# Performance work log

Measured on AMD Instinct MI355X. Metric: run time of the kernel, lower is better.

Reference implementation:

```python
import jax, jax.numpy as jnp
import numpy as np

N_HEAD, DK, DV = 16, 64, 64
TEMP = DK ** 0.5
LN_EPS = 1e-5


def setup_inputs() -> dict:
    key = jax.random.key(0)
    ks = jax.random.split(key, 8)
    B, LQ, LK = 8, 1024, 1024
    D1, D2 = 768, 1024
    return {
        'q': jax.random.normal(ks[0], (B, LQ, D1), jnp.float32),
        'k': jax.random.normal(ks[1], (B, LK, D2), jnp.float32),
        'v': jax.random.normal(ks[2], (B, LK, D2), jnp.float32),
        'w_qs': jax.random.normal(ks[3], (D1, N_HEAD * DK), jnp.float32) * 0.02,
        'w_ks': jax.random.normal(ks[4], (D2, N_HEAD * DK), jnp.float32) * 0.02,
        'w_vs': jax.random.normal(ks[5], (D2, N_HEAD * DV), jnp.float32) * 0.02,
        'fc_w': jax.random.normal(ks[6], (N_HEAD * DV, D2), jnp.float32) * 0.02,
        'resid_w': jax.random.normal(ks[7], (D1, N_HEAD * DV), jnp.float32) * 0.02,
        'resid_b': jnp.zeros((N_HEAD * DV,), jnp.float32),
        'ln_gamma': jnp.ones((D2,), jnp.float32),
        'ln_beta': jnp.zeros((D2,), jnp.float32),
    }


def reference(q, k, v, w_qs, w_ks, w_vs, fc_w, resid_w, resid_b, ln_gamma, ln_beta):
    B, LQ, _ = q.shape
    LK = k.shape[1]
    residual = q
    # project and split heads: [B, L, H, d] -> [B, H, L, d]
    Q = (q @ w_qs).reshape(B, LQ, N_HEAD, DK).transpose(0, 2, 1, 3)
    K = (k @ w_ks).reshape(B, LK, N_HEAD, DK).transpose(0, 2, 1, 3)
    V = (v @ w_vs).reshape(B, LK, N_HEAD, DV).transpose(0, 2, 1, 3)
    scores = jnp.einsum('bhqd,bhkd->bhqk', Q / TEMP, K)
    p = jax.nn.softmax(scores, axis=-1)
    # reverse-complement attention (RCA): reverse=True
    p = (1.0 - p) / (LK - 1)
    out = jnp.einsum('bhqk,bhkd->bhqd', p, V)  # dropout is eval-mode identity
    out = out.transpose(0, 2, 1, 3).reshape(B, LQ, N_HEAD * DV)
    out = out @ fc_w
    out = out + (residual @ resid_w + resid_b)
    mean = jnp.mean(out, axis=-1, keepdims=True)
    var = jnp.var(out, axis=-1, keepdims=True)
    out = (out - mean) * jax.lax.rsqrt(var + LN_EPS) * ln_gamma + ln_beta
    return out  # relu=False
```

## Files before the change

kernel.cpp:

```cpp
#include <hip/hip_runtime.h>

typedef __bf16 bf16_t;
typedef __bf16 bf16x8 __attribute__((ext_vector_type(8)));
typedef __bf16 bf16x4 __attribute__((ext_vector_type(4)));
typedef float  f32x4  __attribute__((ext_vector_type(4)));

#if __has_builtin(__builtin_amdgcn_exp2f)
#define EXP2(x) __builtin_amdgcn_exp2f(x)
#else
#define EXP2(x) exp2f(x)
#endif

#define DEVFN __device__ __forceinline__

DEVFN void gl_lds16(void* lds_base, const void* gsrc) {
  __builtin_amdgcn_global_load_lds(
      (const __attribute__((address_space(1))) void*)gsrc,
      (__attribute__((address_space(3))) void*)lds_base, 16, 0, 0);
}

__global__ __launch_bounds__(256) void k_prep(
    const float* __restrict__ q, const float* __restrict__ k, const float* __restrict__ v,
    const float* __restrict__ w_qs, const float* __restrict__ w_ks,
    const float* __restrict__ w_vs, const float* __restrict__ fc_w,
    const float* __restrict__ resid_w,
    bf16_t* __restrict__ qb, bf16_t* __restrict__ kb, bf16_t* __restrict__ vb,
    bf16_t* __restrict__ wqsT, bf16_t* __restrict__ wksT, bf16_t* __restrict__ wvsT,
    bf16_t* __restrict__ fcwT, bf16_t* __restrict__ rswT,
    float* __restrict__ Vs) {
  __shared__ float t[64][65];
  int bid = blockIdx.x;
  if (bid < 1152) {
    const float* w; bf16_t* wt; int K;
    if (bid < 192)      { w = w_qs;    wt = wqsT; K = 768; }
    else if (bid < 448) { w = w_ks;    wt = wksT; K = 1024; bid -= 192; }
    else if (bid < 704) { w = w_vs;    wt = wvsT; K = 1024; bid -= 448; }
    else if (bid < 960) { w = fc_w;    wt = fcwT; K = 1024; bid -= 704; }
    else                { w = resid_w; wt = rswT; K = 768;  bid -= 960; }
    const int bk = (bid >> 4) << 6;
    const int bn = (bid & 15) << 6;
    const int rr = threadIdx.x >> 4;
    const int cc = (threadIdx.x & 15) << 2;
#pragma unroll
    for (int i = 0; i < 4; ++i) {
      int r = i * 16 + rr;
      float4 vv = *reinterpret_cast<const float4*>(&w[(size_t)(bk + r) * 1024 + bn + cc]);
      t[r][cc] = vv.x; t[r][cc + 1] = vv.y; t[r][cc + 2] = vv.z; t[r][cc + 3] = vv.w;
    }
    __syncthreads();
#pragma unroll
    for (int i = 0; i < 4; ++i) {
      int n = i * 16 + rr;
      bf16x4 o;
      o[0] = (bf16_t)t[cc][n];     o[1] = (bf16_t)t[cc + 1][n];
      o[2] = (bf16_t)t[cc + 2][n]; o[3] = (bf16_t)t[cc + 3][n];
      *reinterpret_cast<bf16x4*>(&wt[(size_t)(bn + n) * K + bk + cc]) = o;
    }
    return;
  }
  bid -= 1152;
  if (bid == 0) {
    for (int j = threadIdx.x; j < 8192; j += 256) Vs[j] = 0.f;
  }
  const int NQ = 1572864, NK = 2097152, NT = NQ + 2 * NK;
  int stride = (gridDim.x - 1152) * 256;
  for (int i = bid * 256 + threadIdx.x; i < NT; i += stride) {
    const float* src; bf16_t* dst; int off;
    if (i < NQ)           { src = q; dst = qb; off = i; }
    else if (i < NQ + NK) { src = k; dst = kb; off = i - NQ; }
    else                  { src = v; dst = vb; off = i - NQ - NK; }
    float4 vv = reinterpret_cast<const float4*>(src)[off];
    bf16x4 o;
    o[0] = (bf16_t)vv.x; o[1] = (bf16_t)vv.y; o[2] = (bf16_t)vv.z; o[3] = (bf16_t)vv.w;
    reinterpret_cast<bf16x4*>(dst)[off] = o;
  }
}

DEVFN void gemm_tiles(const bf16_t* __restrict__ A, const bf16_t* __restrict__ Bt,
                      int K, int m0, int n0, bf16_t (*sm)[4096], f32x4 (&acc)[4][4]) {
  const int lane = threadIdx.x & 63;
  const int wv = threadIdx.x >> 6;
  const int wr = (wv >> 1) * 64, wc = (wv & 1) * 64;
  const int lr = lane & 15, lk = lane >> 4;
  const int so0 = wv * 2048 + lane * 16;
  const int so1 = so0 + 1024;
  const int r0 = so0 >> 6, r1 = so1 >> 6;
  const int c0 = ((((so0 >> 4) & 3) ^ ((r0 >> 1) & 3)) << 4);
  const int c1 = ((((so1 >> 4) & 3) ^ ((r1 >> 1) & 3)) << 4);
  const int asw = ((lk ^ ((lr >> 1) & 3)) << 4);
  const char* Apc = (const char*)A;
  const char* Btc = (const char*)Bt;
  f32x4 zro = {0.f, 0.f, 0.f, 0.f};
#pragma unroll
  for (int i = 0; i < 4; ++i)
#pragma unroll
    for (int j = 0; j < 4; ++j) acc[i][j] = zro;

  const int nk = K >> 5;
  auto stage = [&](int buf, int t) {
    gl_lds16((char*)sm[2 * buf]     + wv * 2048,        Apc + ((size_t)(m0 + r0) * K + t * 32) * 2 + c0);
    gl_lds16((char*)sm[2 * buf]     + wv * 2048 + 1024, Apc + ((size_t)(m0 + r1) * K + t * 32) * 2 + c1);
    gl_lds16((char*)sm[2 * buf + 1] + wv * 2048,        Btc + ((size_t)(n0 + r0) * K + t * 32) * 2 + c0);
    gl_lds16((char*)sm[2 * buf + 1] + wv * 2048 + 1024, Btc + ((size_t)(n0 + r1) * K + t * 32) * 2 + c1);
  };
  stage(0, 0);
  if (nk > 1) {
    stage(1, 1);
    asm volatile("s_waitcnt vmcnt(4)" ::: "memory");
  } else {
    asm volatile("s_waitcnt vmcnt(0)" ::: "memory");
  }
  __builtin_amdgcn_s_barrier();

  for (int t = 0; t < nk; ++t) {
    const int cur = t % 3;
    const char* AsB = (const char*)sm[2 * cur];
    const char* BsB = (const char*)sm[2 * cur + 1];
    bf16x8 af[4], bfr[4];
#pragma unroll
    for (int i = 0; i < 4; ++i)
      af[i] = *(const bf16x8*)(AsB + (wr + i * 16 + lr) * 64 + asw);
#pragma unroll
    for (int j = 0; j < 4; ++j)
      bfr[j] = *(const bf16x8*)(BsB + (wc + j * 16 + lr) * 64 + asw);
#pragma unroll
    for (int i = 0; i < 4; ++i)
#pragma unroll
      for (int j = 0; j < 4; ++j)
        acc[i][j] = __builtin_amdgcn_mfma_f32_16x16x32_bf16(af[i], bfr[j], acc[i][j], 0, 0, 0);
    __builtin_amdgcn_s_barrier();
    if (t + 2 < nk) stage((t + 2) % 3, t + 2);
    if (t + 1 < nk) {
      if (t + 2 < nk) asm volatile("s_waitcnt vmcnt(4)" ::: "memory");
      else            asm volatile("s_waitcnt vmcnt(0)" ::: "memory");
      __builtin_amdgcn_s_barrier();
    }
  }
}

__global__ __launch_bounds__(256, 3) void k_gemm_proj(
    const bf16_t* __restrict__ qb, const bf16_t* __restrict__ wqsT, bf16_t* __restrict__ Qp,
    const bf16_t* __restrict__ kb, const bf16_t* __restrict__ wksT, bf16_t* __restrict__ Kp,
    const bf16_t* __restrict__ vb, const bf16_t* __restrict__ wvsT, bf16_t* __restrict__ Vt,
    float* __restrict__ Vsum, float qscale) {
  __shared__ bf16_t sm[6][4096];
  const int bid = blockIdx.x;
  const int route = bid >> 9;
  const int sbid = bid & 511;
  const int wg = (sbid & 7) * 64 + (sbid >> 3);
  const int tn = 8;
  const int m0 = (wg / tn) << 7;
  const int n0 = (wg % tn) << 7;
  const int lane = threadIdx.x & 63;
  const int wv = threadIdx.x >> 6;
  const int wr = (wv >> 1) * 64, wc = (wv & 1) * 64;
  const int lr = lane & 15, lk = lane >> 4;
  f32x4 acc[4][4];

  if (route == 0) {
    gemm_tiles(vb, wvsT, 1024, m0, n0, sm, acc);
    const int b = m0 >> 10;
    const int h0 = n0 >> 6;
    const int kt0 = (m0 & 1023) >> 6;
    const int h_local = wc >> 6, kt_local = wr >> 6;
    char* tl = (char*)sm + (h_local * 2 + kt_local) * 8192;
#pragma unroll
    for (int i = 0; i < 4; ++i) {
      const int kvl = i * 16 + lk * 4;
      const int csel = kvl >> 3;
      const int hoff = (kvl & 7) * 2;
#pragma unroll
      for (int j = 0; j < 4; ++j) {
        const int d = j * 16 + lr;
        bf16x4 pw;
#pragma unroll
        for (int r = 0; r < 4; ++r) pw[r] = (bf16_t)acc[i][j][r];
        *reinterpret_cast<bf16x4*>(tl + d * 128 + ((csel ^ (d & 7)) << 4) + hoff) = pw;
      }
    }
    {
      const size_t gbase = (size_t)(b * 16 + h0 + h_local) * 131072 +
                           (size_t)(kt0 + kt_local) * 8192;
#pragma unroll
      for (int it = 0; it < 8; ++it)
        *reinterpret_cast<uint4*>((char*)Vt + gbase + it * 1024 + lane * 16) =
            *reinterpret_cast<const uint4*>(tl + it * 1024 + lane * 16);
    }
    const int h = h0 + h_local;
#pragma unroll
    for (int j = 0; j < 4; ++j) {
      float s = 0.f;
#pragma unroll
      for (int i = 0; i < 4; ++i)
#pragma unroll
        for (int r = 0; r < 4; ++r) s += acc[i][j][r];
      s += __shfl_xor(s, 16, 64);
      s += __shfl_xor(s, 32, 64);
      if (lane < 16)
        atomicAdd(&Vsum[(b * 16 + h) * 64 + j * 16 + lane], s);
    }
  } else if (route == 1) {
    gemm_tiles(kb, wksT, 1024, m0, n0, sm, acc);
#pragma unroll
    for (int i = 0; i < 4; ++i)
#pragma unroll
      for (int j = 0; j < 4; ++j)
#pragma unroll
        for (int r = 0; r < 4; ++r)
          Kp[(size_t)(m0 + wr + i * 16 + lk * 4 + r) * 1024 + n0 + wc + j * 16 + lr] =
              (bf16_t)acc[i][j][r];
  } else {
    gemm_tiles(qb, wqsT, 768, m0, n0, sm, acc);
#pragma unroll
    for (int i = 0; i < 4; ++i)
#pragma unroll
      for (int j = 0; j < 4; ++j)
#pragma unroll
        for (int r = 0; r < 4; ++r)
          Qp[(size_t)(m0 + wr + i * 16 + lk * 4 + r) * 1024 + n0 + wc + j * 16 + lr] =
              (bf16_t)(acc[i][j][r] * qscale);
  }
}

__global__ __launch_bounds__(256, 3) void k_gemm_final(
    const bf16_t* __restrict__ A1, const bf16_t* __restrict__ B1t, int K1,
    const bf16_t* __restrict__ A2, const bf16_t* __restrict__ B2t, int K2,
    const float* __restrict__ bias, bf16_t* __restrict__ Y, int N) {
  __shared__ bf16_t sm[6][4096];
  const int bpx = gridDim.x >> 3;
  const int wg = (blockIdx.x & 7) * bpx + (blockIdx.x >> 3);
  const int tn = N >> 7;
  const int m0 = (wg / tn) << 7;
  const int n0 = (wg % tn) << 7;
  const int lane = threadIdx.x & 63;
  const int wv = threadIdx.x >> 6;
  const int wr = (wv >> 1) * 64, wc = (wv & 1) * 64;
  const int lr = lane & 15, lk = lane >> 4;
  const int so0 = wv * 2048 + lane * 16;
  const int so1 = so0 + 1024;
  const int r0 = so0 >> 6, r1 = so1 >> 6;
  const int c0 = ((((so0 >> 4) & 3) ^ ((r0 >> 1) & 3)) << 4);
  const int c1 = ((((so1 >> 4) & 3) ^ ((r1 >> 1) & 3)) << 4);
  const int asw = ((lk ^ ((lr >> 1) & 3)) << 4);
  f32x4 zro = {0.f, 0.f, 0.f, 0.f};
  f32x4 acc[4][4];
#pragma unroll
  for (int i = 0; i < 4; ++i)
#pragma unroll
    for (int j = 0; j < 4; ++j) acc[i][j] = zro;

  const int nk1 = K1 >> 5;
  const int nkt = (K1 + K2) >> 5;
  auto stage = [&](int buf, int t) {
    const char* Apc; const char* Btc; int K, tt;
    if (t < nk1) { Apc = (const char*)A1; Btc = (const char*)B1t; K = K1; tt = t; }
    else         { Apc = (const char*)A2; Btc = (const char*)B2t; K = K2; tt = t - nk1; }
    gl_lds16((char*)sm[2 * buf]     + wv * 2048,        Apc + ((size_t)(m0 + r0) * K + tt * 32) * 2 + c0);
    gl_lds16((char*)sm[2 * buf]     + wv * 2048 + 1024, Apc + ((size_t)(m0 + r1) * K + tt * 32) * 2 + c1);
    gl_lds16((char*)sm[2 * buf + 1] + wv * 2048,        Btc + ((size_t)(n0 + r0) * K + tt * 32) * 2 + c0);
    gl_lds16((char*)sm[2 * buf + 1] + wv * 2048 + 1024, Btc + ((size_t)(n0 + r1) * K + tt * 32) * 2 + c1);
  };
  stage(0, 0);
  stage(1, 1);
  asm volatile("s_waitcnt vmcnt(4)" ::: "memory");
  __builtin_amdgcn_s_barrier();
  for (int t = 0; t < nkt; ++t) {
    const int cur = t % 3;
    const char* AsB = (const char*)sm[2 * cur];
    const char* BsB = (const char*)sm[2 * cur + 1];
    bf16x8 af[4], bfr[4];
#pragma unroll
    for (int i = 0; i < 4; ++i)
      af[i] = *(const bf16x8*)(AsB + (wr + i * 16 + lr) * 64 + asw);
#pragma unroll
    for (int j = 0; j < 4; ++j)
      bfr[j] = *(const bf16x8*)(BsB + (wc + j * 16 + lr) * 64 + asw);
#pragma unroll
    for (int i = 0; i < 4; ++i)
#pragma unroll
      for (int j = 0; j < 4; ++j)
        acc[i][j] = __builtin_amdgcn_mfma_f32_16x16x32_bf16(af[i], bfr[j], acc[i][j], 0, 0, 0);
    __builtin_amdgcn_s_barrier();
    if (t + 2 < nkt) stage((t + 2) % 3, t + 2);
    if (t + 1 < nkt) {
      if (t + 2 < nkt) asm volatile("s_waitcnt vmcnt(4)" ::: "memory");
      else             asm volatile("s_waitcnt vmcnt(0)" ::: "memory");
      __builtin_amdgcn_s_barrier();
    }
  }
#pragma unroll
  for (int i = 0; i < 4; ++i)
#pragma unroll
    for (int j = 0; j < 4; ++j) {
      float bv = bias[n0 + wc + j * 16 + lr];
#pragma unroll
      for (int r = 0; r < 4; ++r)
        Y[(size_t)(m0 + wr + i * 16 + lk * 4 + r) * N + n0 + wc + j * 16 + lr] =
            (bf16_t)(acc[i][j][r] + bv);
    }
}

__global__ __launch_bounds__(1024) void k_attn(
    const bf16_t* __restrict__ Qp, const bf16_t* __restrict__ Kp,
    const bf16_t* __restrict__ Vt, const float* __restrict__ Vsum,
    bf16_t* __restrict__ Aout) {
  const int bid = blockIdx.x;
  const int wgid = (bid & 7) * 32 + (bid >> 3);
  const int qg = wgid & 1;
  const int bh = wgid >> 1;
  const int b = bh >> 4, h = bh & 15;
  __shared__ bf16_t Ks[2][4096];
  __shared__ bf16_t Vs[2][4096];
  const int tid = threadIdx.x;
  const int lane = tid & 63;
  const int wv = tid >> 6;
  const int lr = lane & 15, lk = lane >> 4;
  const int stb = (wv >> 2) * 2;
  const int wrow = (wv & 3) * 16;

  const int o = (tid & 511) * 16;
  const int row = o >> 7;
  const int sc = ((((o >> 4) & 7) ^ (row & 7)) << 4);
  const int srow = (row & 0x23) | ((row & 0x0C) << 1) | ((row & 0x10) >> 2);
  const bool isK = tid < 512;

  const char* Ksrc  = (const char*)(Kp + ((size_t)(b * 1024 + srow)) * 1024 + h * 64) + sc;
  const char* Vtile = (const char*)Vt + (size_t)bh * 131072 + o;
  const char* gsrc   = isK ? Ksrc : Vtile;
  const size_t gstep = isK ? (size_t)131072 : (size_t)8192;
  char* l0 = isK ? ((char*)&Ks[0][0] + o) : ((char*)&Vs[0][0] + o);
  char* l1 = isK ? ((char*)&Ks[1][0] + o) : ((char*)&Vs[1][0] + o);

  gl_lds16(l0, gsrc);

  bf16x8 qa[2][2];
#pragma unroll
  for (int stl = 0; stl < 2; ++stl) {
    const char* qsrc = (const char*)(Qp +
        ((size_t)(b * 1024 + qg * 512 + (stb + stl) * 64 + wrow + lr)) * 1024 + h * 64);
    qa[stl][0] = *(const bf16x8*)(qsrc + lk * 16);
    qa[stl][1] = *(const bf16x8*)(qsrc + 64 + lk * 16);
  }
  __syncthreads();

  const int kb0 = lr * 128 + ((lk ^ (lr & 7)) << 4);
  const int kb1 = lr * 128 + (((4 + lk) ^ (lr & 7)) << 4);

  f32x4 zro = {0.f, 0.f, 0.f, 0.f};
  f32x4 oacc[2][4];
  f32x4 sum[2];
#pragma unroll
  for (int stl = 0; stl < 2; ++stl) {
    sum[stl] = zro;
#pragma unroll
    for (int g = 0; g < 4; ++g) oacc[stl][g] = zro;
  }
  bf16x8 ones8;
#pragma unroll
  for (int j = 0; j < 8; ++j) ones8[j] = (bf16_t)1.0f;

  for (int kt = 0; kt < 16; ++kt) {
    const int cur = kt & 1;
    const char* KsB = (const char*)&Ks[cur][0];
    const char* VsB = (const char*)&Vs[cur][0];
    if (kt < 15)
      gl_lds16(cur ? l0 : l1, gsrc + (size_t)(kt + 1) * gstep);

    f32x4 sacc[2][4];
#pragma unroll
    for (int stl = 0; stl < 2; ++stl)
#pragma unroll
      for (int g = 0; g < 4; ++g) sacc[stl][g] = zro;
    {
      bf16x8 kf[4];
#pragma unroll
      for (int g = 0; g < 4; ++g) kf[g] = *(const bf16x8*)(KsB + kb0 + g * 2048);
#pragma unroll
      for (int stl = 0; stl < 2; ++stl)
#pragma unroll
        for (int g = 0; g < 4; ++g)
          sacc[stl][g] = __builtin_amdgcn_mfma_f32_16x16x32_bf16(kf[g], qa[stl][0], sacc[stl][g], 0, 0, 0);
#pragma unroll
      for (int g = 0; g < 4; ++g) kf[g] = *(const bf16x8*)(KsB + kb1 + g * 2048);
#pragma unroll
      for (int stl = 0; stl < 2; ++stl)
#pragma unroll
        for (int g = 0; g < 4; ++g)
          sacc[stl][g] = __builtin_amdgcn_mfma_f32_16x16x32_bf16(kf[g], qa[stl][1], sacc[stl][g], 0, 0, 0);
    }

    bf16x8 pa[2][2];
#pragma unroll
    for (int stl = 0; stl < 2; ++stl)
#pragma unroll
      for (int c = 0; c < 2; ++c) {
        bf16x8 pw;
#pragma unroll
        for (int r = 0; r < 4; ++r) {
          pw[r]     = (bf16_t)EXP2(sacc[stl][2 * c][r]);
          pw[4 + r] = (bf16_t)EXP2(sacc[stl][2 * c + 1][r]);
        }
        pa[stl][c] = pw;
      }

#pragma unroll
    for (int c = 0; c < 2; ++c) {
      const int vb = (c == 0) ? kb0 : kb1;
      bf16x8 vf[4];
#pragma unroll
      for (int gd = 0; gd < 4; ++gd)
        vf[gd] = *(const bf16x8*)(VsB + vb + gd * 2048);
#pragma unroll
      for (int stl = 0; stl < 2; ++stl) {
        sum[stl] = __builtin_amdgcn_mfma_f32_16x16x32_bf16(pa[stl][c], ones8, sum[stl], 0, 0, 0);
#pragma unroll
        for (int gd = 0; gd < 4; ++gd)
          oacc[stl][gd] = __builtin_amdgcn_mfma_f32_16x16x32_bf16(pa[stl][c], vf[gd], oacc[stl][gd], 0, 0, 0);
      }
    }
    __syncthreads();
  }

  float vs_d[4];
#pragma unroll
  for (int gd = 0; gd < 4; ++gd) vs_d[gd] = Vsum[bh * 64 + gd * 16 + lr];
#pragma unroll
  for (int stl = 0; stl < 2; ++stl) {
    float inv[4];
#pragma unroll
    for (int r = 0; r < 4; ++r) inv[r] = 1.0f / sum[stl][r];
#pragma unroll
    for (int gd = 0; gd < 4; ++gd)
#pragma unroll
      for (int r = 0; r < 4; ++r) {
        int d = gd * 16 + lr;
        int qrow = qg * 512 + (stb + stl) * 64 + wrow + lk * 4 + r;
        float attnv = oacc[stl][gd][r] * inv[r];
        float val = (vs_d[gd] - attnv) * (1.0f / 1023.0f);
        Aout[((size_t)(b * 1024 + qrow)) * 1024 + h * 64 + d] = (bf16_t)val;
      }
  }
}

__global__ __launch_bounds__(256) void k_ln(
    const bf16_t* __restrict__ Y, const float* __restrict__ gamma,
    const float* __restrict__ beta, float* __restrict__ out) {
  const int row = blockIdx.x, tid = threadIdx.x;
  bf16x4 xv = reinterpret_cast<const bf16x4*>(Y + (size_t)row * 1024)[tid];
  float x0 = (float)xv[0], x1 = (float)xv[1], x2 = (float)xv[2], x3 = (float)xv[3];
  float s = x0 + x1 + x2 + x3;
  float q = x0 * x0 + x1 * x1 + x2 * x2 + x3 * x3;
#pragma unroll
  for (int off = 32; off > 0; off >>= 1) {
    s += __shfl_xor(s, off, 64);
    q += __shfl_xor(q, off, 64);
  }
  __shared__ float ss[4], qs[4];
  if ((tid & 63) == 0) { ss[tid >> 6] = s; qs[tid >> 6] = q; }
  __syncthreads();
  s = ss[0] + ss[1] + ss[2] + ss[3];
  q = qs[0] + qs[1] + qs[2] + qs[3];
  float mean = s * (1.f / 1024.f);
  float var = q * (1.f / 1024.f) - mean * mean;
  float rstd = rsqrtf(var + 1e-5f);
  float4 g = reinterpret_cast<const float4*>(gamma)[tid];
  float4 bt = reinterpret_cast<const float4*>(beta)[tid];
  float4 o;
  o.x = (x0 - mean) * rstd * g.x + bt.x;
  o.y = (x1 - mean) * rstd * g.y + bt.y;
  o.z = (x2 - mean) * rstd * g.z + bt.z;
  o.w = (x3 - mean) * rstd * g.w + bt.w;
  reinterpret_cast<float4*>(out + (size_t)row * 1024)[tid] = o;
}

extern "C" void kernel_launch(void* const* d_in, const int* in_sizes, int n_in,
                              void* d_out, int out_size, void* d_ws, size_t ws_size,
                              hipStream_t stream) {
  (void)in_sizes; (void)n_in; (void)out_size;
  const float* q       = (const float*)d_in[0];
  const float* k       = (const float*)d_in[1];
  const float* v       = (const float*)d_in[2];
  const float* w_qs    = (const float*)d_in[3];
  const float* w_ks    = (const float*)d_in[4];
  const float* w_vs    = (const float*)d_in[5];
  const float* fc_w    = (const float*)d_in[6];
  const float* resid_w = (const float*)d_in[7];
  const float* resid_b = (const float*)d_in[8];
  const float* ln_g    = (const float*)d_in[9];
  const float* ln_b    = (const float*)d_in[10];
  float* out = (float*)d_out;
  char* ws = (char*)d_ws;

  if (ws_size < (size_t)122716160) return;

  bf16_t* qb   = (bf16_t*)(ws + 0);
  bf16_t* kb   = (bf16_t*)(ws + 12582912);
  bf16_t* vb   = (bf16_t*)(ws + 29360128);
  bf16_t* Y    = (bf16_t*)(ws + 12582912);
  bf16_t* wqsT = (bf16_t*)(ws + 46137344);
  bf16_t* wksT = (bf16_t*)(ws + 47710208);
  bf16_t* wvsT = (bf16_t*)(ws + 49807360);
  bf16_t* fcwT = (bf16_t*)(ws + 51904512);
  bf16_t* rswT = (bf16_t*)(ws + 54001664);
  bf16_t* Qp   = (bf16_t*)(ws + 55574528);
  bf16_t* Kp   = (bf16_t*)(ws + 72351744);
  bf16_t* Aout = (bf16_t*)(ws + 89128960);
  bf16_t* VtT  = (bf16_t*)(ws + 105906176);
  float*  Vsm  = (float*)(ws + 122683392);

  k_prep<<<3200, 256, 0, stream>>>(q, k, v, w_qs, w_ks, w_vs, fc_w, resid_w,
                                   qb, kb, vb, wqsT, wksT, wvsT, fcwT, rswT, Vsm);
  k_gemm_proj<<<1536, 256, 0, stream>>>(qb, wqsT, Qp, kb, wksT, Kp, vb, wvsT, VtT,
                                        Vsm, 0.18033688011f);
  k_attn<<<256, 1024, 0, stream>>>(Qp, Kp, VtT, Vsm, Aout);
  k_gemm_final<<<512, 256, 0, stream>>>(Aout, fcwT, 1024, qb, rswT, 768, resid_b, Y, 1024);
  k_ln<<<8192, 256, 0, stream>>>(Y, ln_g, ln_b, out);
}
```

Baseline: 168.1 us.

## Enlarge GEMM tiles to 256x128 for projection and final GEMMs

Doubles the M dimension of the GEMM block tile from 128 to 256 rows in both the projection and final GEMM kernels. Each wave now computes 128x64 with 8x4 MFMA accumulators, and staging loads 4 A and 2 B chunks per thread into a larger 72KB triple-buffered LDS. The V-transpose epilogue is reworked to write two 64-row tiles per wave. This raises arithmetic intensity and halves the grid, but increases register and LDS pressure and drops the occupancy hint. The final GEMM now gets only 256 blocks, which may underfill the GPU.

Result: slower. 200.9 us (+19.5%).

```diff
diff --git a/kernel.cpp b/kernel.cpp
--- a/kernel.cpp
+++ b/kernel.cpp
@@ -77,121 +77,134 @@
 }
 
 DEVFN void gemm_tiles(const bf16_t* __restrict__ A, const bf16_t* __restrict__ Bt,
-                      int K, int m0, int n0, bf16_t (*sm)[4096], f32x4 (&acc)[4][4]) {
-  const int lane = threadIdx.x & 63;
-  const int wv = threadIdx.x >> 6;
-  const int wr = (wv >> 1) * 64, wc = (wv & 1) * 64;
+                      int K, int m0, int n0, char* sm, f32x4 (&acc)[8][4]) {
+  const int tid = threadIdx.x;
+  const int lane = tid & 63;
+  const int wv = tid >> 6;
+  const int wr = (wv >> 1) * 128, wc = (wv & 1) * 64;
   const int lr = lane & 15, lk = lane >> 4;
-  const int so0 = wv * 2048 + lane * 16;
-  const int so1 = so0 + 1024;
-  const int r0 = so0 >> 6, r1 = so1 >> 6;
-  const int c0 = ((((so0 >> 4) & 3) ^ ((r0 >> 1) & 3)) << 4);
-  const int c1 = ((((so1 >> 4) & 3) ^ ((r1 >> 1) & 3)) << 4);
   const int asw = ((lk ^ ((lr >> 1) & 3)) << 4);
   const char* Apc = (const char*)A;
   const char* Btc = (const char*)Bt;
+
+  int rA[4], cA[4], rB[2], cB[2];
+#pragma unroll
+  for (int it = 0; it < 4; ++it) {
+    int o = tid * 16 + it * 4096;
+    rA[it] = o >> 6;
+    cA[it] = ((((o >> 4) & 3) ^ ((rA[it] >> 1) & 3)) << 4);
+  }
+#pragma unroll
+  for (int it = 0; it < 2; ++it) {
+    int o = tid * 16 + it * 4096;
+    rB[it] = o >> 6;
+    cB[it] = ((((o >> 4) & 3) ^ ((rB[it] >> 1) & 3)) << 4);
+  }
+
   f32x4 zro = {0.f, 0.f, 0.f, 0.f};
 #pragma unroll
-  for (int i = 0; i < 4; ++i)
+  for (int i = 0; i < 8; ++i)
 #pragma unroll
     for (int j = 0; j < 4; ++j) acc[i][j] = zro;
 
   const int nk = K >> 5;
   auto stage = [&](int buf, int t) {
-    gl_lds16((char*)sm[2 * buf]     + wv * 2048,        Apc + ((size_t)(m0 + r0) * K + t * 32) * 2 + c0);
-    gl_lds16((char*)sm[2 * buf]     + wv * 2048 + 1024, Apc + ((size_t)(m0 + r1) * K + t * 32) * 2 + c1);
-    gl_lds16((char*)sm[2 * buf + 1] + wv * 2048,        Btc + ((size_t)(n0 + r0) * K + t * 32) * 2 + c0);
-    gl_lds16((char*)sm[2 * buf + 1] + wv * 2048 + 1024, Btc + ((size_t)(n0 + r1) * K + t * 32) * 2 + c1);
+    char* base = sm + buf * 24576;
+#pragma unroll
+    for (int it = 0; it < 4; ++it)
+      gl_lds16(base + tid * 16 + it * 4096,
+               Apc + ((size_t)(m0 + rA[it]) * K + t * 32) * 2 + cA[it]);
+#pragma unroll
+    for (int it = 0; it < 2; ++it)
+      gl_lds16(base + 16384 + tid * 16 + it * 4096,
+               Btc + ((size_t)(n0 + rB[it]) * K + t * 32) * 2 + cB[it]);
   };
   stage(0, 0);
-  if (nk > 1) {
-    stage(1, 1);
-    asm volatile("s_waitcnt vmcnt(4)" ::: "memory");
-  } else {
-    asm volatile("s_waitcnt vmcnt(0)" ::: "memory");
-  }
+  stage(1, 1);
+  asm volatile("s_waitcnt vmcnt(6)" ::: "memory");
   __builtin_amdgcn_s_barrier();
 
   for (int t = 0; t < nk; ++t) {
     const int cur = t % 3;
-    const char* AsB = (const char*)sm[2 * cur];
-    const char* BsB = (const char*)sm[2 * cur + 1];
-    bf16x8 af[4], bfr[4];
-#pragma unroll
-    for (int i = 0; i < 4; ++i)
+    const char* AsB = sm + cur * 24576;
+    const char* BsB = AsB + 16384;
+    bf16x8 af[8], bfr[4];
+#pragma unroll
+    for (int i = 0; i < 8; ++i)
       af[i] = *(const bf16x8*)(AsB + (wr + i * 16 + lr) * 64 + asw);
 #pragma unroll
     for (int j = 0; j < 4; ++j)
       bfr[j] = *(const bf16x8*)(BsB + (wc + j * 16 + lr) * 64 + asw);
 #pragma unroll
-    for (int i = 0; i < 4; ++i)
+    for (int i = 0; i < 8; ++i)
 #pragma unroll
       for (int j = 0; j < 4; ++j)
         acc[i][j] = __builtin_amdgcn_mfma_f32_16x16x32_bf16(af[i], bfr[j], acc[i][j], 0, 0, 0);
     __builtin_amdgcn_s_barrier();
     if (t + 2 < nk) stage((t + 2) % 3, t + 2);
     if (t + 1 < nk) {
-      if (t + 2 < nk) asm volatile("s_waitcnt vmcnt(4)" ::: "memory");
+      if (t + 2 < nk) asm volatile("s_waitcnt vmcnt(6)" ::: "memory");
       else            asm volatile("s_waitcnt vmcnt(0)" ::: "memory");
       __builtin_amdgcn_s_barrier();
     }
   }
 }
 
-__global__ __launch_bounds__(256, 3) void k_gemm_proj(
+__global__ __launch_bounds__(256) void k_gemm_proj(
     const bf16_t* __restrict__ qb, const bf16_t* __restrict__ wqsT, bf16_t* __restrict__ Qp,
     const bf16_t* __restrict__ kb, const bf16_t* __restrict__ wksT, bf16_t* __restrict__ Kp,
     const bf16_t* __restrict__ vb, const bf16_t* __restrict__ wvsT, bf16_t* __restrict__ Vt,
     float* __restrict__ Vsum, float qscale) {
-  __shared__ bf16_t sm[6][4096];
+  __shared__ __align__(16) char sm[73728];
   const int bid = blockIdx.x;
-  const int route = bid >> 9;
-  const int sbid = bid & 511;
-  const int wg = (sbid & 7) * 64 + (sbid >> 3);
-  const int tn = 8;
-  const int m0 = (wg / tn) << 7;
-  const int n0 = (wg % tn) << 7;
+  const int route = bid >> 8;
+  const int sbid = bid & 255;
+  const int wg = (sbid & 7) * 32 + (sbid >> 3);
+  const int m0 = (wg >> 3) << 8;
+  const int n0 = (wg & 7) << 7;
   const int lane = threadIdx.x & 63;
   const int wv = threadIdx.x >> 6;
-  const int wr = (wv >> 1) * 64, wc = (wv & 1) * 64;
+  const int wr = (wv >> 1) * 128, wc = (wv & 1) * 64;
   const int lr = lane & 15, lk = lane >> 4;
-  f32x4 acc[4][4];
+  f32x4 acc[8][4];
 
   if (route == 0) {
     gemm_tiles(vb, wvsT, 1024, m0, n0, sm, acc);
     const int b = m0 >> 10;
     const int h0 = n0 >> 6;
     const int kt0 = (m0 & 1023) >> 6;
-    const int h_local = wc >> 6, kt_local = wr >> 6;
-    char* tl = (char*)sm + (h_local * 2 + kt_local) * 8192;
-#pragma unroll
-    for (int i = 0; i < 4; ++i) {
-      const int kvl = i * 16 + lk * 4;
+    const int h_local = wc >> 6;
+#pragma unroll
+    for (int i = 0; i < 8; ++i) {
+      const int kvl = (i & 3) * 16 + lk * 4;
       const int csel = kvl >> 3;
       const int hoff = (kvl & 7) * 2;
+      char* slot = sm + (wv * 2 + (i >> 2)) * 8192;
 #pragma unroll
       for (int j = 0; j < 4; ++j) {
         const int d = j * 16 + lr;
         bf16x4 pw;
 #pragma unroll
         for (int r = 0; r < 4; ++r) pw[r] = (bf16_t)acc[i][j][r];
-        *reinterpret_cast<bf16x4*>(tl + d * 128 + ((csel ^ (d & 7)) << 4) + hoff) = pw;
+        *reinterpret_cast<bf16x4*>(slot + d * 128 + ((csel ^ (d & 7)) << 4) + hoff) = pw;
       }
     }
     {
-      const size_t gbase = (size_t)(b * 16 + h0 + h_local) * 131072 +
-                           (size_t)(kt0 + kt_local) * 8192;
-#pragma unroll
-      for (int it = 0; it < 8; ++it)
-        *reinterpret_cast<uint4*>((char*)Vt + gbase + it * 1024 + lane * 16) =
-            *reinterpret_cast<const uint4*>(tl + it * 1024 + lane * 16);
+      const size_t gb = (size_t)(b * 16 + h0 + h_local) * 131072 +
+                        (size_t)(kt0 + (wr >> 6)) * 8192;
+#pragma unroll
+      for (int tl = 0; tl < 2; ++tl)
+#pragma unroll
+        for (int it = 0; it < 8; ++it)
+          *reinterpret_cast<uint4*>((char*)Vt + gb + tl * 8192 + it * 1024 + lane * 16) =
+              *reinterpret_cast<const uint4*>(sm + (wv * 2 + tl) * 8192 + it * 1024 + lane * 16);
     }
     const int h = h0 + h_local;
 #pragma unroll
     for (int j = 0; j < 4; ++j) {
       float s = 0.f;
 #pragma unroll
-      for (int i = 0; i < 4; ++i)
+      for (int i = 0; i < 8; ++i)
 #pragma unroll
         for (int r = 0; r < 4; ++r) s += acc[i][j][r];
       s += __shfl_xor(s, 16, 64);
@@ -202,7 +215,7 @@
   } else if (route == 1) {
     gemm_tiles(kb, wksT, 1024, m0, n0, sm, acc);
 #pragma unroll
-    for (int i = 0; i < 4; ++i)
+    for (int i = 0; i < 8; ++i)
 #pragma unroll
       for (int j = 0; j < 4; ++j)
 #pragma unroll
@@ -212,7 +225,7 @@
   } else {
     gemm_tiles(qb, wqsT, 768, m0, n0, sm, acc);
 #pragma unroll
-    for (int i = 0; i < 4; ++i)
+    for (int i = 0; i < 8; ++i)
 #pragma unroll
       for (int j = 0; j < 4; ++j)
 #pragma unroll
@@ -222,30 +235,40 @@
   }
 }
 
-__global__ __launch_bounds__(256, 3) void k_gemm_final(
+__global__ __launch_bounds__(256) void k_gemm_final(
     const bf16_t* __restrict__ A1, const bf16_t* __restrict__ B1t, int K1,
     const bf16_t* __restrict__ A2, const bf16_t* __restrict__ B2t, int K2,
     const float* __restrict__ bias, bf16_t* __restrict__ Y, int N) {
-  __shared__ bf16_t sm[6][4096];
-  const int bpx = gridDim.x >> 3;
-  const int wg = (blockIdx.x & 7) * bpx + (blockIdx.x >> 3);
-  const int tn = N >> 7;
-  const int m0 = (wg / tn) << 7;
-  const int n0 = (wg % tn) << 7;
-  const int lane = threadIdx.x & 63;
-  const int wv = threadIdx.x >> 6;
-  const int wr = (wv >> 1) * 64, wc = (wv & 1) * 64;
+  __shared__ __align__(16) char sm[73728];
+  const int bid = blockIdx.x;
+  const int wg = (bid & 7) * 32 + (bid >> 3);
+  const int m0 = (wg >> 3) << 8;
+  const int n0 = (wg & 7) << 7;
+  const int tid = threadIdx.x;
+  const int lane = tid & 63;
+  const int wv = tid >> 6;
+  const int wr = (wv >> 1) * 128, wc = (wv & 1) * 64;
   const int lr = lane & 15, lk = lane >> 4;
-  const int so0 = wv * 2048 + lane * 16;
-  const int so1 = so0 + 1024;
-  const int r0 = so0 >> 6, r1 = so1 >> 6;
-  const int c0 = ((((so0 >> 4) & 3) ^ ((r0 >> 1) & 3)) << 4);
-  const int c1 = ((((so1 >> 4) & 3) ^ ((r1 >> 1) & 3)) << 4);
   const int asw = ((lk ^ ((lr >> 1) & 3)) << 4);
+
+  int rA[4], cA[4], rB[2], cB[2];
+#pragma unroll
+  for (int it = 0; it < 4; ++it) {
+    int o = tid * 16 + it * 4096;
+    rA[it] = o >> 6;
+    cA[it] = ((((o >> 4) & 3) ^ ((rA[it] >> 1) & 3)) << 4);
+  }
+#pragma unroll
+  for (int it = 0; it < 2; ++it) {
+    int o = tid * 16 + it * 4096;
+    rB[it] = o >> 6;
+    cB[it] = ((((o >> 4) & 3) ^ ((rB[it] >> 1) & 3)) << 4);
+  }
+
   f32x4 zro = {0.f, 0.f, 0.f, 0.f};
-  f32x4 acc[4][4];
-#pragma unroll
-  for (int i = 0; i < 4; ++i)
+  f32x4 acc[8][4];
+#pragma unroll
+  for (int i = 0; i < 8; ++i)
 #pragma unroll
     for (int j = 0; j < 4; ++j) acc[i][j] = zro;
 
@@ -255,41 +278,46 @@
     const char* Apc; const char* Btc; int K, tt;
     if (t < nk1) { Apc = (const char*)A1; Btc = (const char*)B1t; K = K1; tt = t; }
     else         { Apc = (const char*)A2; Btc = (const char*)B2t; K = K2; tt = t - nk1; }
-    gl_lds16((char*)sm[2 * buf]     + wv * 2048,        Apc + ((size_t)(m0 + r0) * K + tt * 32) * 2 + c0);
-    gl_lds16((char*)sm[2 * buf]     + wv * 2048 + 1024, Apc + ((size_t)(m0 + r1) * K + tt * 32) * 2 + c1);
-    gl_lds16((char*)sm[2 * buf + 1] + wv * 2048,        Btc + ((size_t)(n0 + r0) * K + tt * 32) * 2 + c0);
-    gl_lds16((char*)sm[2 * buf + 1] + wv * 2048 + 1024, Btc + ((size_t)(n0 + r1) * K + tt * 32) * 2 + c1);
+    char* base = sm + buf * 24576;
+#pragma unroll
+    for (int it = 0; it < 4; ++it)
+      gl_lds16(base + tid * 16 + it * 4096,
+               Apc + ((size_t)(m0 + rA[it]) * K + tt * 32) * 2 + cA[it]);
+#pragma unroll
+    for (int it = 0; it < 2; ++it)
+      gl_lds16(base + 16384 + tid * 16 + it * 4096,
+               Btc + ((size_t)(n0 + rB[it]) * K + tt * 32) * 2 + cB[it]);
   };
   stage(0, 0);
   stage(1, 1);
-  asm volatile("s_waitcnt vmcnt(4)" ::: "memory");
+  asm volatile("s_waitcnt vmcnt(6)" ::: "memory");
   __builtin_amdgcn_s_barrier();
   for (int t = 0; t < nkt; ++t) {
     const int cur = t % 3;
-    const char* AsB = (const char*)sm[2 * cur];
-    const char* BsB = (const char*)sm[2 * cur + 1];
-    bf16x8 af[4], bfr[4];
-#pragma unroll
-    for (int i = 0; i < 4; ++i)
+    const char* AsB = sm + cur * 24576;
+    const char* BsB = AsB + 16384;
+    bf16x8 af[8], bfr[4];
+#pragma unroll
+    for (int i = 0; i < 8; ++i)
       af[i] = *(const bf16x8*)(AsB + (wr + i * 16 + lr) * 64 + asw);
 #pragma unroll
     for (int j = 0; j < 4; ++j)
       bfr[j] = *(const bf16x8*)(BsB + (wc + j * 16 + lr) * 64 + asw);
 #pragma unroll
-    for (int i = 0; i < 4; ++i)
+    for (int i = 0; i < 8; ++i)
 #pragma unroll
       for (int j = 0; j < 4; ++j)
         acc[i][j] = __builtin_amdgcn_mfma_f32_16x16x32_bf16(af[i], bfr[j], acc[i][j], 0, 0, 0);
     __builtin_amdgcn_s_barrier();
     if (t + 2 < nkt) stage((t + 2) % 3, t + 2);
     if (t + 1 < nkt) {
-      if (t + 2 < nkt) asm volatile("s_waitcnt vmcnt(4)" ::: "memory");
+      if (t + 2 < nkt) asm volatile("s_waitcnt vmcnt(6)" ::: "memory");
       else             asm volatile("s_waitcnt vmcnt(0)" ::: "memory");
       __builtin_amdgcn_s_barrier();
     }
   }
 #pragma unroll
-  for (int i = 0; i < 4; ++i)
+  for (int i = 0; i < 8; ++i)
 #pragma unroll
     for (int j = 0; j < 4; ++j) {
       float bv = bias[n0 + wc + j * 16 + lr];
@@ -510,9 +538,9 @@
 
   k_prep<<<3200, 256, 0, stream>>>(q, k, v, w_qs, w_ks, w_vs, fc_w, resid_w,
                                    qb, kb, vb, wqsT, wksT, wvsT, fcwT, rswT, Vsm);
-  k_gemm_proj<<<1536, 256, 0, stream>>>(qb, wqsT, Qp, kb, wksT, Kp, vb, wvsT, VtT,
-                                        Vsm, 0.18033688011f);
+  k_gemm_proj<<<768, 256, 0, stream>>>(qb, wqsT, Qp, kb, wksT, Kp, vb, wvsT, VtT,
+                                       Vsm, 0.18033688011f);
   k_attn<<<256, 1024, 0, stream>>>(Qp, Kp, VtT, Vsm, Aout);
-  k_gemm_final<<<512, 256, 0, stream>>>(Aout, fcwT, 1024, qb, rswT, 768, resid_b, Y, 1024);
+  k_gemm_final<<<256, 256, 0, stream>>>(Aout, fcwT, 1024, qb, rswT, 768, resid_b, Y, 1024);
   k_ln<<<8192, 256, 0, stream>>>(Y, ln_g, ln_b, out);
 }
```

## Fuse fp32-to-bf16 conversion of k and v into projection GEMM A-loads

Applied to the files above, without the earlier changes.

The prep kernel no longer converts the k and v inputs to bf16. The projection GEMM for K and V gets a new tile routine that reads the fp32 A-tiles into registers, converts them, and writes them to LDS. The B operand still uses direct global-to-LDS loads, with a three-stage buffer and register double-buffering for A. This removes a full write and re-read of about 32 MB of bf16 intermediates, but doubles the A-side global traffic inside the GEMM and adds conversion and LDS-store work to its inner loop.

Result: slower. 177.8 us (+5.8%).

```diff
diff --git a/kernel.cpp b/kernel.cpp
--- a/kernel.cpp
+++ b/kernel.cpp
@@ -20,11 +20,11 @@
 }
 
 __global__ __launch_bounds__(256) void k_prep(
-    const float* __restrict__ q, const float* __restrict__ k, const float* __restrict__ v,
+    const float* __restrict__ q,
     const float* __restrict__ w_qs, const float* __restrict__ w_ks,
     const float* __restrict__ w_vs, const float* __restrict__ fc_w,
     const float* __restrict__ resid_w,
-    bf16_t* __restrict__ qb, bf16_t* __restrict__ kb, bf16_t* __restrict__ vb,
+    bf16_t* __restrict__ qb,
     bf16_t* __restrict__ wqsT, bf16_t* __restrict__ wksT, bf16_t* __restrict__ wvsT,
     bf16_t* __restrict__ fcwT, bf16_t* __restrict__ rswT,
     float* __restrict__ Vs) {
@@ -62,17 +62,13 @@
   if (bid == 0) {
     for (int j = threadIdx.x; j < 8192; j += 256) Vs[j] = 0.f;
   }
-  const int NQ = 1572864, NK = 2097152, NT = NQ + 2 * NK;
+  const int NQ = 1572864;
   int stride = (gridDim.x - 1152) * 256;
-  for (int i = bid * 256 + threadIdx.x; i < NT; i += stride) {
-    const float* src; bf16_t* dst; int off;
-    if (i < NQ)           { src = q; dst = qb; off = i; }
-    else if (i < NQ + NK) { src = k; dst = kb; off = i - NQ; }
-    else                  { src = v; dst = vb; off = i - NQ - NK; }
-    float4 vv = reinterpret_cast<const float4*>(src)[off];
+  for (int i = bid * 256 + threadIdx.x; i < NQ; i += stride) {
+    float4 vv = reinterpret_cast<const float4*>(q)[i];
     bf16x4 o;
     o[0] = (bf16_t)vv.x; o[1] = (bf16_t)vv.y; o[2] = (bf16_t)vv.z; o[3] = (bf16_t)vv.w;
-    reinterpret_cast<bf16x4*>(dst)[off] = o;
+    reinterpret_cast<bf16x4*>(qb)[i] = o;
   }
 }
 
@@ -138,10 +134,101 @@
   }
 }
 
+DEVFN void gemm_tiles_f32(const float* __restrict__ Af, const bf16_t* __restrict__ Bt,
+                          int K, int m0, int n0, bf16_t (*sm)[4096], f32x4 (&acc)[4][4]) {
+  const int tid = threadIdx.x;
+  const int lane = tid & 63;
+  const int wv = tid >> 6;
+  const int wr = (wv >> 1) * 64, wc = (wv & 1) * 64;
+  const int lr = lane & 15, lk = lane >> 4;
+  const int asw = ((lk ^ ((lr >> 1) & 3)) << 4);
+  const int so0 = wv * 2048 + lane * 16;
+  const int so1 = so0 + 1024;
+  const int r0 = so0 >> 6, r1 = so1 >> 6;
+  const int c0 = ((((so0 >> 4) & 3) ^ ((r0 >> 1) & 3)) << 4);
+  const int c1 = ((((so1 >> 4) & 3) ^ ((r1 >> 1) & 3)) << 4);
+  const char* Btc = (const char*)Bt;
+  const int ar = tid >> 1, ach = tid & 1;
+  const int s4 = (ar >> 1) & 3;
+  const int offA0 = ar * 64 + (((2 * ach)     ^ s4) << 4);
+  const int offA1 = ar * 64 + (((2 * ach + 1) ^ s4) << 4);
+  const float* abase = Af + (size_t)(m0 + ar) * K + ach * 16;
+
+  f32x4 zro = {0.f, 0.f, 0.f, 0.f};
+#pragma unroll
+  for (int i = 0; i < 4; ++i)
+#pragma unroll
+    for (int j = 0; j < 4; ++j) acc[i][j] = zro;
+
+  const int nk = K >> 5;
+  f32x4 rE[4], rO[4];
+
+  auto loadA = [&](f32x4 (&r)[4], int t) {
+    const f32x4* p = (const f32x4*)(abase + t * 32);
+    r[0] = p[0]; r[1] = p[1]; r[2] = p[2]; r[3] = p[3];
+  };
+  auto stageB = [&](int buf, int t) {
+    gl_lds16((char*)sm[2 * buf + 1] + wv * 2048,        Btc + ((size_t)(n0 + r0) * K + t * 32) * 2 + c0);
+    gl_lds16((char*)sm[2 * buf + 1] + wv * 2048 + 1024, Btc + ((size_t)(n0 + r1) * K + t * 32) * 2 + c1);
+  };
+  auto writeA = [&](int buf, f32x4 (&r)[4]) {
+    bf16x8 w0, w1;
+#pragma unroll
+    for (int j = 0; j < 4; ++j) {
+      w0[j] = (bf16_t)r[0][j]; w0[4 + j] = (bf16_t)r[1][j];
+      w1[j] = (bf16_t)r[2][j]; w1[4 + j] = (bf16_t)r[3][j];
+    }
+    char* bufA = (char*)sm[2 * buf];
+    *reinterpret_cast<bf16x8*>(bufA + offA0) = w0;
+    *reinterpret_cast<bf16x8*>(bufA + offA1) = w1;
+  };
+
+  loadA(rE, 0); stageB(0, 0);
+  loadA(rO, 1); stageB(1, 1);
+  asm volatile("s_waitcnt vmcnt(6)" ::: "memory");
+  writeA(0, rE);
+  asm volatile("s_waitcnt lgkmcnt(0)" ::: "memory");
+  __builtin_amdgcn_s_barrier();
+
+  auto compute = [&](int u) {
+    const int cur = u % 3;
+    const char* AsB = (const char*)sm[2 * cur];
+    const char* BsB = (const char*)sm[2 * cur + 1];
+    bf16x8 af[4], bfr[4];
+#pragma unroll
+    for (int i = 0; i < 4; ++i)
+      af[i] = *(const bf16x8*)(AsB + (wr + i * 16 + lr) * 64 + asw);
+#pragma unroll
+    for (int j = 0; j < 4; ++j)
+      bfr[j] = *(const bf16x8*)(BsB + (wc + j * 16 + lr) * 64 + asw);
+#pragma unroll
+    for (int i = 0; i < 4; ++i)
+#pragma unroll
+      for (int j = 0; j < 4; ++j)
+        acc[i][j] = __builtin_amdgcn_mfma_f32_16x16x32_bf16(af[i], bfr[j], acc[i][j], 0, 0, 0);
+    __builtin_amdgcn_s_barrier();
+  };
+  auto publish = [&](int u, f32x4 (&rNew)[4], f32x4 (&rWr)[4]) {
+    if (u + 2 < nk) { loadA(rNew, u + 2); stageB((u + 2) % 3, u + 2); }
+    if (u + 1 < nk) {
+      if (u + 2 < nk) asm volatile("s_waitcnt vmcnt(6)" ::: "memory");
+      else            asm volatile("s_waitcnt vmcnt(0)" ::: "memory");
+      writeA((u + 1) % 3, rWr);
+      asm volatile("s_waitcnt lgkmcnt(0)" ::: "memory");
+      __builtin_amdgcn_s_barrier();
+    }
+  };
+
+  for (int t = 0; t < nk; t += 2) {
+    compute(t);     publish(t, rE, rO);
+    compute(t + 1); publish(t + 1, rO, rE);
+  }
+}
+
 __global__ __launch_bounds__(256, 3) void k_gemm_proj(
     const bf16_t* __restrict__ qb, const bf16_t* __restrict__ wqsT, bf16_t* __restrict__ Qp,
-    const bf16_t* __restrict__ kb, const bf16_t* __restrict__ wksT, bf16_t* __restrict__ Kp,
-    const bf16_t* __restrict__ vb, const bf16_t* __restrict__ wvsT, bf16_t* __restrict__ Vt,
+    const float* __restrict__ kf, const bf16_t* __restrict__ wksT, bf16_t* __restrict__ Kp,
+    const float* __restrict__ vf, const bf16_t* __restrict__ wvsT, bf16_t* __restrict__ Vt,
     float* __restrict__ Vsum, float qscale) {
   __shared__ bf16_t sm[6][4096];
   const int bid = blockIdx.x;
@@ -158,7 +245,7 @@
   f32x4 acc[4][4];
 
   if (route == 0) {
-    gemm_tiles(vb, wvsT, 1024, m0, n0, sm, acc);
+    gemm_tiles_f32(vf, wvsT, 1024, m0, n0, sm, acc);
     const int b = m0 >> 10;
     const int h0 = n0 >> 6;
     const int kt0 = (m0 & 1023) >> 6;
@@ -200,7 +287,7 @@
         atomicAdd(&Vsum[(b * 16 + h) * 64 + j * 16 + lane], s);
     }
   } else if (route == 1) {
-    gemm_tiles(kb, wksT, 1024, m0, n0, sm, acc);
+    gemm_tiles_f32(kf, wksT, 1024, m0, n0, sm, acc);
 #pragma unroll
     for (int i = 0; i < 4; ++i)
 #pragma unroll
@@ -372,21 +459,21 @@
 #pragma unroll
       for (int g = 0; g < 4; ++g) sacc[stl][g] = zro;
     {
-      bf16x8 kf[4];
-#pragma unroll
-      for (int g = 0; g < 4; ++g) kf[g] = *(const bf16x8*)(KsB + kb0 + g * 2048);
+      bf16x8 kf2[4];
+#pragma unroll
+      for (int g = 0; g < 4; ++g) kf2[g] = *(const bf16x8*)(KsB + kb0 + g * 2048);
 #pragma unroll
       for (int stl = 0; stl < 2; ++stl)
 #pragma unroll
         for (int g = 0; g < 4; ++g)
-          sacc[stl][g] = __builtin_amdgcn_mfma_f32_16x16x32_bf16(kf[g], qa[stl][0], sacc[stl][g], 0, 0, 0);
-#pragma unroll
-      for (int g = 0; g < 4; ++g) kf[g] = *(const bf16x8*)(KsB + kb1 + g * 2048);
+          sacc[stl][g] = __builtin_amdgcn_mfma_f32_16x16x32_bf16(kf2[g], qa[stl][0], sacc[stl][g], 0, 0, 0);
+#pragma unroll
+      for (int g = 0; g < 4; ++g) kf2[g] = *(const bf16x8*)(KsB + kb1 + g * 2048);
 #pragma unroll
       for (int stl = 0; stl < 2; ++stl)
 #pragma unroll
         for (int g = 0; g < 4; ++g)
-          sacc[stl][g] = __builtin_amdgcn_mfma_f32_16x16x32_bf16(kf[g], qa[stl][1], sacc[stl][g], 0, 0, 0);
+          sacc[stl][g] = __builtin_amdgcn_mfma_f32_16x16x32_bf16(kf2[g], qa[stl][1], sacc[stl][g], 0, 0, 0);
     }
 
     bf16x8 pa[2][2];
@@ -406,16 +493,16 @@
 #pragma unroll
     for (int c = 0; c < 2; ++c) {
       const int vb = (c == 0) ? kb0 : kb1;
-      bf16x8 vf[4];
+      bf16x8 vf2[4];
 #pragma unroll
       for (int gd = 0; gd < 4; ++gd)
-        vf[gd] = *(const bf16x8*)(VsB + vb + gd * 2048);
+        vf2[gd] = *(const bf16x8*)(VsB + vb + gd * 2048);
 #pragma unroll
       for (int stl = 0; stl < 2; ++stl) {
         sum[stl] = __builtin_amdgcn_mfma_f32_16x16x32_bf16(pa[stl][c], ones8, sum[stl], 0, 0, 0);
 #pragma unroll
         for (int gd = 0; gd < 4; ++gd)
-          oacc[stl][gd] = __builtin_amdgcn_mfma_f32_16x16x32_bf16(pa[stl][c], vf[gd], oacc[stl][gd], 0, 0, 0);
+          oacc[stl][gd] = __builtin_amdgcn_mfma_f32_16x16x32_bf16(pa[stl][c], vf2[gd], oacc[stl][gd], 0, 0, 0);
       }
     }
     __syncthreads();
@@ -494,8 +581,6 @@
   if (ws_size < (size_t)122716160) return;
 
   bf16_t* qb   = (bf16_t*)(ws + 0);
-  bf16_t* kb   = (bf16_t*)(ws + 12582912);
-  bf16_t* vb   = (bf16_t*)(ws + 29360128);
   bf16_t* Y    = (bf16_t*)(ws + 12582912);
   bf16_t* wqsT = (bf16_t*)(ws + 46137344);
   bf16_t* wksT = (bf16_t*)(ws + 47710208);
@@ -508,9 +593,9 @@
   bf16_t* VtT  = (bf16_t*)(ws + 105906176);
   float*  Vsm  = (float*)(ws + 122683392);
 
-  k_prep<<<3200, 256, 0, stream>>>(q, k, v, w_qs, w_ks, w_vs, fc_w, resid_w,
-                                   qb, kb, vb, wqsT, wksT, wvsT, fcwT, rswT, Vsm);
-  k_gemm_proj<<<1536, 256, 0, stream>>>(qb, wqsT, Qp, kb, wksT, Kp, vb, wvsT, VtT,
+  k_prep<<<1920, 256, 0, stream>>>(q, w_qs, w_ks, w_vs, fc_w, resid_w,
+                                   qb, wqsT, wksT, wvsT, fcwT, rswT, Vsm);
+  k_gemm_proj<<<1536, 256, 0, stream>>>(qb, wqsT, Qp, k, wksT, Kp, v, wvsT, VtT,
                                         Vsm, 0.18033688011f);
   k_attn<<<256, 1024, 0, stream>>>(Qp, Kp, VtT, Vsm, Aout);
   k_gemm_final<<<512, 256, 0, stream>>>(Aout, fcwT, 1024, qb, rswT, 768, resid_b, Y, 1024);
```
